# Kernel optimization log

Hardware: AMD Instinct MI355X
Metric: run time of the kernel (lower is better)

The kernel has to match this reference:

```python
import jax, jax.numpy as jnp
import numpy as np

B, T, P, D, H = 32, 64, 196, 768, 12
HD = D // H   # MHA head dim = 64
F = D // H    # GAT per-head out features = 64


def _grid_adj(num_patches):
    g = int(np.sqrt(num_patches))
    a = np.zeros((num_patches, num_patches), np.int32)
    for i in range(num_patches):
        a[i, i] = 1
        r, c = divmod(i, g)
        for dr in (-1, 0, 1):
            for dc in (-1, 0, 1):
                if dr == 0 and dc == 0:
                    continue
                nr, nc = r + dr, c + dc
                if 0 <= nr < g and 0 <= nc < g:
                    a[i, nr * g + nc] = 1
    return a


def setup_inputs():
    key = jax.random.key(0)
    ks = jax.random.split(key, 32)
    s = 0.02
    ta = jax.random.randint(ks[2], (B, T, T), 0, 2).astype(jnp.int32)
    ta = jnp.maximum(jnp.maximum(ta, ta.transpose(0, 2, 1)), jnp.eye(T, dtype=jnp.int32))
    return {
        'text_features': jax.random.normal(ks[0], (B, T, D), jnp.float32),
        'image_features': jax.random.normal(ks[1], (B, P, D), jnp.float32),
        'clip_text': jax.random.normal(ks[3], (B, 512), jnp.float32),
        'clip_image': jax.random.normal(ks[4], (B, 512), jnp.float32),
        'logit_scale': jnp.float32(4.6052),  # ln(100), CLIP default
        'wq': jax.random.normal(ks[5], (D, D), jnp.float32) * s,
        'bq': jnp.zeros((D,), jnp.float32),
        'wk': jax.random.normal(ks[6], (D, D), jnp.float32) * s,
        'bk': jnp.zeros((D,), jnp.float32),
        'wv': jax.random.normal(ks[7], (D, D), jnp.float32) * s,
        'bv': jnp.zeros((D,), jnp.float32),
        'wo': jax.random.normal(ks[8], (D, D), jnp.float32) * s,
        'bo': jnp.zeros((D,), jnp.float32),
        'Wt': jax.random.normal(ks[9], (D, H * F), jnp.float32) * s,
        'at': jax.random.normal(ks[10], (2 * F, 1), jnp.float32) * s,
        'Wi': jax.random.normal(ks[11], (D, H * F), jnp.float32) * s,
        'ai': jax.random.normal(ks[12], (2 * F, 1), jnp.float32) * s,
        'Wp': jax.random.normal(ks[13], (512, D), jnp.float32) * s,
        'bp': jnp.zeros((D,), jnp.float32),
        'f1w': jax.random.normal(ks[14], (3, 16), jnp.float32) * 0.3,
        'f1b': jnp.zeros((16,), jnp.float32),
        'f2w': jax.random.normal(ks[15], (16, 3), jnp.float32) * 0.3,
        'f2b': jnp.zeros((3,), jnp.float32),
        'c1w': jax.random.normal(ks[16], (D, D // 2), jnp.float32) * s,
        'c1b': jnp.zeros((D // 2,), jnp.float32),
        'c2w': jax.random.normal(ks[17], (D // 2, 2), jnp.float32) * s,
        'c2b': jnp.zeros((2,), jnp.float32),
        'text_adj': ta,
        'image_adj': jnp.asarray(_grid_adj(P)),
    }


def _gat(h, adj, W, a):
    # h: [N, D], adj: [N, N] (0/1), W: [D, H*F], a: [2F, 1]
    N = h.shape[0]
    Wh = (h @ W).reshape(N, H, F)
    # e_ij = leakyrelu(a^T [Wh_i ; Wh_j]) decomposed to avoid the N*N*2F concat tensor
    src = jnp.einsum('nhf,f->nh', Wh, a[:F, 0])   # [N, H]
    dst = jnp.einsum('nhf,f->nh', Wh, a[F:, 0])   # [N, H]
    e = jax.nn.leaky_relu(src[:, None, :] + dst[None, :, :], 0.2)  # [N, N, H]
    e = jnp.where(adj[:, :, None] > 0, e, jnp.float32(-9e15))
    att = jax.nn.softmax(e, axis=1)               # softmax over neighbors j
    hp = jnp.einsum('ijh,jhf->ihf', att, Wh)       # [N, H, F]
    return jax.nn.elu(hp.reshape(N, H * F))


def reference(text_features, image_features, clip_text, clip_image, logit_scale,
              wq, bq, wk, bk, wv, bv, wo, bo, Wt, at, Wi, ai, Wp, bp,
              f1w, f1b, f2w, f2b, c1w, c1b, c2w, c2b, text_adj, image_adj):
    # token-level cross attention (text queries, image keys/values)
    q = (text_features @ wq + bq).reshape(B, T, H, HD)
    k = (image_features @ wk + bk).reshape(B, P, H, HD)
    v = (image_features @ wv + bv).reshape(B, P, H, HD)
    scores = jnp.einsum('bthd,bphd->bhtp', q, k) / jnp.sqrt(jnp.float32(HD))
    upd = jnp.einsum('bhtp,bphd->bthd', jax.nn.softmax(scores, axis=-1), v)
    upd = upd.reshape(B, T, D) @ wo + bo           # [B, T, D]
    c = jnp.einsum('btd,bpd->btp', upd, image_features)
    s_token = jnp.mean(jnp.diagonal(c, axis1=-2, axis2=-1), axis=1)  # [B]
    f_token = upd.mean(axis=1)                     # [B, D]
    # per-sample GATs, batched via vmap
    tg = jax.vmap(lambda h, a_: _gat(h, a_, Wt, at))(text_features, text_adj)
    ig = jax.vmap(lambda h: _gat(h, image_adj, Wi, ai))(image_features)
    tgf = tg.mean(axis=1)
    igf = ig.mean(axis=1)

    def cos(x, y):
        nx = jnp.maximum(jnp.linalg.norm(x, axis=-1), 1e-8)
        ny = jnp.maximum(jnp.linalg.norm(y, axis=-1), 1e-8)
        return jnp.sum(x * y, axis=-1) / (nx * ny)

    s_phrase = cos(tgf, igf)
    s_global = jnp.exp(logit_scale) * cos(clip_text, clip_image)
    f_global = clip_text @ Wp + bp
    scores3 = jax.lax.stop_gradient(jnp.stack([s_token, s_phrase, s_global], axis=1))
    w = jax.nn.sigmoid(jax.nn.gelu(scores3 @ f1w + f1b, approximate=False) @ f2w + f2b)
    f_agg = w[:, 0:1] * f_token + w[:, 1:2] * tgf + w[:, 2:3] * f_global
    logits = jax.nn.relu(f_agg @ c1w + c1b) @ c2w + c2b  # dropout inactive (eval)
    return logits
```

## Files before the change

### kernel.cpp

```cpp
#include <hip/hip_runtime.h>
#include <hip/hip_bf16.h>
#include <math.h>

#define B 32
#define T 64
#define P 196
#define D 768
#define H 12

typedef __attribute__((ext_vector_type(8))) short short8;
typedef __attribute__((ext_vector_type(4))) float floatx4;

__device__ __forceinline__ float wave_sum(float v) {
#pragma unroll
  for (int o = 32; o > 0; o >>= 1) v += __shfl_xor(v, o);
  return v;
}
__device__ __forceinline__ unsigned short f2bf(float x) {
  unsigned u = __float_as_uint(x);
  u += 0x7FFFu + ((u >> 16) & 1u);
  return (unsigned short)(u >> 16);
}
__device__ __forceinline__ float bf2f(unsigned short x) {
  return __uint_as_float((unsigned)x << 16);
}
__device__ __forceinline__ float fexp(float x) { return __expf(x); }
__device__ __forceinline__ float frcp(float x) { return __builtin_amdgcn_rcpf(x); }
__device__ __forceinline__ void async_cp16(const unsigned short* g, unsigned short* l) {
  __builtin_amdgcn_global_load_lds(
      (const __attribute__((address_space(1))) unsigned int*)g,
      (__attribute__((address_space(3))) unsigned int*)l, 16, 0, 0);
}
__device__ __forceinline__ int xcd_remap(int orig, int nwg) {
  const int q = nwg >> 3, r = nwg & 7;
  const int x = orig & 7, o = orig >> 3;
  return (x < r ? x * (q + 1) : r * (q + 1) + (x - r) * q) + o;
}

struct WPack {
  const float* src[6];
  unsigned short* dst[6];
};
__global__ __launch_bounds__(256) void prep_kernel(
    WPack p,
    const float* __restrict__ text, unsigned short* __restrict__ text_bf, int n40,
    const float* __restrict__ img, unsigned short* __restrict__ img_bf, int n41,
    const float* __restrict__ bq, const float* __restrict__ bk,
    const float* __restrict__ bv,
    float* __restrict__ bt, float* __restrict__ bi, float* __restrict__ stok,
    const float* __restrict__ clip_t, const float* __restrict__ Wp,
    const float* __restrict__ bp, float* __restrict__ fglob) {
  const int bid = blockIdx.x;
  if (bid < 3456) {
    __shared__ float tile[32][33];
    const int z = bid / 576, rem = bid % 576;
    const int bx = rem % 24, by = rem / 24;
    const float* W = p.src[z];
    unsigned short* Wt = p.dst[z];
    const int tx = threadIdx.x & 31, ty = threadIdx.x >> 5;
    const int n0 = bx * 32, k0 = by * 32;
#pragma unroll
    for (int r = 0; r < 4; ++r)
      tile[ty + 8 * r][tx] = W[(size_t)(k0 + ty + 8 * r) * D + n0 + tx];
    __syncthreads();
#pragma unroll
    for (int r = 0; r < 4; ++r)
      Wt[(size_t)(n0 + ty + 8 * r) * D + k0 + tx] = f2bf(tile[tx][ty + 8 * r]);
  } else if (bid < 9696) {
    int i = (bid - 3456) * 256 + threadIdx.x;
    const float* X;
    unsigned short* Y;
    int idx;
    if (i < n40) { X = text; Y = text_bf; idx = i; }
    else if (i < n40 + n41) { X = img; Y = img_bf; idx = i - n40; }
    else return;
    float4 vv = ((const float4*)X)[idx];
    ushort4 o;
    o.x = f2bf(vv.x); o.y = f2bf(vv.y); o.z = f2bf(vv.z); o.w = f2bf(vv.w);
    ((ushort4*)Y)[idx] = o;
  } else if (bid < 9708) {
    int i = (bid - 9696) * 256 + threadIdx.x;
    if (i < 32) stok[i] = 0.f;
    if (i < 768) { bt[i] = bq[i]; bi[i] = bk[i]; }
    else if (i < 1536) { bt[i] = 0.f; bi[i] = bv[i - 768]; }
    else if (i < 2304) { bi[i] = 0.f; }
  } else {
    __shared__ float red[4][64];
    const int bid2 = bid - 9708;
    const int jt = bid2 % 12, b = bid2 / 12;
    const int j = threadIdx.x & 63, kc = threadIdx.x >> 6;
    const float* ct = clip_t + b * 512 + kc * 128;
    const float* wp = Wp + (size_t)(kc * 128) * D + jt * 64 + j;
    float s0 = 0.f, s1 = 0.f, s2 = 0.f, s3 = 0.f;
#pragma unroll
    for (int k = 0; k < 128; k += 4) {
      s0 += ct[k]     * wp[(size_t)k * D];
      s1 += ct[k + 1] * wp[(size_t)(k + 1) * D];
      s2 += ct[k + 2] * wp[(size_t)(k + 2) * D];
      s3 += ct[k + 3] * wp[(size_t)(k + 3) * D];
    }
    red[kc][j] = (s0 + s1) + (s2 + s3);
    __syncthreads();
    if (kc == 0)
      fglob[b * D + jt * 64 + j] =
          red[0][j] + red[1][j] + red[2][j] + red[3][j] + bp[jt * 64 + j];
  }
}

struct GemmJob {
  const unsigned short* A;
  const unsigned short* Bt;
  const float* bias;
  void* C;
  int N, K, lda, ldb, colTiles;
};

template <bool BF16OUT>
__device__ __forceinline__ void gemm_body(const GemmJob& j, int bx, int by, int tid) {
  __shared__ unsigned short As[3][128][32];
  __shared__ unsigned short Bs[3][128][32];
  const int lane = tid & 63;
  const int w = tid >> 6;
  const int quad = lane >> 4;
  const int l15 = lane & 15;
  const int row0 = by * 128;
  const int col0 = bx * 128;
  const int m_off = (w & 1) * 64;
  const int n_off = (w >> 1) * 64;
  const int N = j.N, K = j.K;

  const int srow = 16 * w + (lane >> 2);
  const int scol = (((lane & 3) ^ ((lane >> 3) & 3))) * 8;
  const unsigned short* gA0 = j.A + (size_t)(row0 + srow) * j.lda + scol;
  const unsigned short* gA1 = j.A + (size_t)(row0 + srow + 64) * j.lda + scol;
  const unsigned short* gB0 = j.Bt + (size_t)(col0 + srow) * j.ldb + scol;
  const unsigned short* gB1 = j.Bt + (size_t)(col0 + srow + 64) * j.ldb + scol;

  const int rdc = (quad ^ ((l15 >> 1) & 3)) * 8;

  floatx4 acc[4][4] = {};
  short8 fA[4], fB_[4];
  short8 gA_[4], gB_[4];

#define STAGE(buf, kk)                                   \
  do {                                                   \
    async_cp16(gA0 + (kk), &As[buf][16 * w][0]);         \
    async_cp16(gA1 + (kk), &As[buf][64 + 16 * w][0]);    \
    async_cp16(gB0 + (kk), &Bs[buf][16 * w][0]);         \
    async_cp16(gB1 + (kk), &Bs[buf][64 + 16 * w][0]);    \
  } while (0)

  auto RD = [&](short8 (&AF)[4], short8 (&BF)[4], int buf) {
#pragma unroll
    for (int i = 0; i < 4; ++i)
      AF[i] = *(const short8*)&As[buf][m_off + 16 * i + l15][rdc];
#pragma unroll
    for (int j2 = 0; j2 < 4; ++j2)
      BF[j2] = *(const short8*)&Bs[buf][n_off + 16 * j2 + l15][rdc];
  };
  auto MM = [&](short8 (&AF)[4], short8 (&BF)[4]) {
#pragma unroll
    for (int i = 0; i < 4; ++i)
#pragma unroll
      for (int j2 = 0; j2 < 4; ++j2)
        acc[i][j2] = __builtin_amdgcn_mfma_f32_16x16x32_bf16(AF[i], BF[j2], acc[i][j2], 0, 0, 0);
  };
  auto PHASE = [&](short8 (&curA)[4], short8 (&curB)[4],
                   short8 (&nxtA)[4], short8 (&nxtB)[4],
                   int stageBuf, int readBuf, int kk) {
    if (kk + 64 < K) {
      STAGE(stageBuf, kk + 64);
      asm volatile("s_waitcnt vmcnt(4) lgkmcnt(0)" ::: "memory");
      __builtin_amdgcn_s_barrier();
      __builtin_amdgcn_sched_barrier(0);
      RD(nxtA, nxtB, readBuf);
    } else if (kk + 32 < K) {
      asm volatile("s_waitcnt vmcnt(0) lgkmcnt(0)" ::: "memory");
      __builtin_amdgcn_s_barrier();
      __builtin_amdgcn_sched_barrier(0);
      RD(nxtA, nxtB, readBuf);
    }
    MM(curA, curB);
  };

  STAGE(0, 0);
  STAGE(1, 32);
  asm volatile("s_waitcnt vmcnt(4)" ::: "memory");
  __builtin_amdgcn_s_barrier();
  __builtin_amdgcn_sched_barrier(0);
  RD(fA, fB_, 0);

  for (int k0 = 0; k0 < K; k0 += 192) {
    PHASE(fA, fB_, gA_, gB_, 2, 1, k0);
    PHASE(gA_, gB_, fA, fB_, 0, 2, k0 + 32);
    PHASE(fA, fB_, gA_, gB_, 1, 0, k0 + 64);
    PHASE(gA_, gB_, fA, fB_, 2, 1, k0 + 96);
    PHASE(fA, fB_, gA_, gB_, 0, 2, k0 + 128);
    PHASE(gA_, gB_, fA, fB_, 1, 0, k0 + 160);
  }
#undef STAGE

#pragma unroll
  for (int jj = 0; jj < 4; ++jj) {
    const int cg = col0 + n_off + 16 * jj + l15;
    const float bv = j.bias ? j.bias[cg] : 0.0f;
#pragma unroll
    for (int i = 0; i < 4; ++i) {
      const int rbase = row0 + m_off + 16 * i + quad * 4;
#pragma unroll
      for (int r = 0; r < 4; ++r) {
        const float val = acc[i][jj][r] + bv;
        const size_t idx = (size_t)(rbase + r) * N + cg;
        if (BF16OUT) ((unsigned short*)j.C)[idx] = f2bf(val);
        else ((float*)j.C)[idx] = val;
      }
    }
  }
}

__global__ __launch_bounds__(256) void gemm_mfma_dual_bf16(GemmJob j0, GemmJob j1,
                                                           int split, int total) {
  const bool first = ((int)blockIdx.x < split);
  const GemmJob& j = first ? j0 : j1;
  const int orig = first ? blockIdx.x : (blockIdx.x - split);
  const int bid = xcd_remap(orig, first ? split : total - split);
  const int bx = bid % j.colTiles;
  const int by = bid / j.colTiles;
  gemm_body<true>(j, bx, by, threadIdx.x);
}

__global__ __launch_bounds__(256) void gemm_mfma_quad_f32(GemmJob j0, GemmJob j1,
                                                          GemmJob j2, GemmJob j3,
                                                          int per) {
  const int which = (int)blockIdx.x / per;
  const GemmJob& j = (which == 0) ? j0 : (which == 1) ? j1 : (which == 2) ? j2 : j3;
  const int orig = (int)blockIdx.x - which * per;
  const int bid = xcd_remap(orig, per);
  const int bx = bid % j.colTiles;
  const int by = bid / j.colTiles;
  gemm_body<false>(j, bx, by, threadIdx.x);
}


__device__ __forceinline__ void attn_body(
    char* smem, int h, int b,
    const unsigned short* __restrict__ qa, const unsigned short* __restrict__ kvw,
    unsigned short* __restrict__ attout) {
  const int tid = threadIdx.x, lane = tid & 63, w = tid >> 6;
  const int quad = lane >> 4, l15 = lane & 15;

  unsigned short (*Ks)[72] = (unsigned short(*)[72])smem;
  unsigned short (*Ps)[16][232] = (unsigned short(*)[16][232])smem;
  unsigned short (*VT)[232] = (unsigned short(*)[232])(smem + 29952);

  short8 aq[2];
#pragma unroll
  for (int ks = 0; ks < 2; ++ks)
    aq[ks] = *(const short8*)(qa + (size_t)(b * T + 16 * w + l15) * 1536 + h * 64 +
                              32 * ks + quad * 8);

  for (int i = tid; i < P * 8; i += 256) {
    const int p = i >> 3, dg = i & 7;
    const short8 k8 =
        *(const short8*)(kvw + (size_t)(b * P + p) * 2304 + h * 64 + dg * 8);
    *(short8*)&Ks[p][dg * 8] = k8;
  }
  {
    const int d = lane;
    const unsigned short* vbase = kvw + (size_t)b * P * 2304 + 768 + h * 64 + d;
    for (int pb = w; pb < 28; pb += 4) {
      short8 v;
#pragma unroll
      for (int z = 0; z < 8; ++z) {
        const int p = pb * 8 + z;
        v[z] = (p < P) ? (short)vbase[(size_t)p * 2304] : (short)0;
      }
      *(short8*)&VT[d][pb * 8] = v;
    }
  }
  __syncthreads();

  floatx4 sc[13];
#pragma unroll
  for (int tile = 0; tile < 13; ++tile) {
    int p = tile * 16 + l15;
    if (p > 195) p = 195;
    short8 bk0 = *(const short8*)&Ks[p][quad * 8];
    short8 bk1 = *(const short8*)&Ks[p][32 + quad * 8];
    floatx4 c = {};
    c = __builtin_amdgcn_mfma_f32_16x16x32_bf16(aq[0], bk0, c, 0, 0, 0);
    c = __builtin_amdgcn_mfma_f32_16x16x32_bf16(aq[1], bk1, c, 0, 0, 0);
    sc[tile] = c;
  }

  float mx[4] = {-3.4e38f, -3.4e38f, -3.4e38f, -3.4e38f};
#pragma unroll
  for (int tile = 0; tile < 13; ++tile)
#pragma unroll
    for (int r = 0; r < 4; ++r) {
      float s = sc[tile][r] * 0.125f;
      if (tile == 12 && l15 >= 4) s = -3.0e38f;
      sc[tile][r] = s;
      mx[r] = fmaxf(mx[r], s);
    }
#pragma unroll
  for (int off = 1; off < 16; off <<= 1)
#pragma unroll
    for (int r = 0; r < 4; ++r) mx[r] = fmaxf(mx[r], __shfl_xor(mx[r], off));

  float sm[4] = {};
#pragma unroll
  for (int tile = 0; tile < 13; ++tile)
#pragma unroll
    for (int r = 0; r < 4; ++r) {
      float e = fexp(sc[tile][r] - mx[r]);
      sc[tile][r] = e;
      sm[r] += e;
    }
#pragma unroll
  for (int off = 1; off < 16; off <<= 1)
#pragma unroll
    for (int r = 0; r < 4; ++r) sm[r] += __shfl_xor(sm[r], off);
  float inv[4];
#pragma unroll
  for (int r = 0; r < 4; ++r) inv[r] = frcp(sm[r]);

  __syncthreads();

#pragma unroll
  for (int tile = 0; tile < 13; ++tile)
#pragma unroll
    for (int r = 0; r < 4; ++r)
      Ps[w][quad * 4 + r][tile * 16 + l15] = f2bf(sc[tile][r]);
#pragma unroll
  for (int r = 0; r < 4; ++r)
    Ps[w][quad * 4 + r][208 + l15] = 0;

  floatx4 oc[4] = {};
#pragma unroll
  for (int ks = 0; ks < 7; ++ks) {
    short8 pa = *(const short8*)&Ps[w][l15][ks * 32 + quad * 8];
#pragma unroll
    for (int nt = 0; nt < 4; ++nt) {
      short8 bv = *(const short8*)&VT[nt * 16 + l15][ks * 32 + quad * 8];
      oc[nt] = __builtin_amdgcn_mfma_f32_16x16x32_bf16(pa, bv, oc[nt], 0, 0, 0);
    }
  }

#pragma unroll
  for (int nt = 0; nt < 4; ++nt)
#pragma unroll
    for (int r = 0; r < 4; ++r)
      attout[(size_t)(b * T + 16 * w + quad * 4 + r) * 768 + h * 64 + nt * 16 + l15] =
          f2bf(oc[nt][r] * inv[r]);
}

__device__ __forceinline__ void text_gat_body(
    char* smem, int h, int b,
    const unsigned short* __restrict__ Wh, int ldw, const int* __restrict__ adj,
    const float* __restrict__ at, float* __restrict__ tgf) {
  const int tid = threadIdx.x, lane = tid & 63, w = tid >> 6;
  const int quad = lane >> 4, l15 = lane & 15;

  unsigned short (*VT)[72] = (unsigned short(*)[72])smem;
  unsigned short (*Ps)[16][72] = (unsigned short(*)[16][72])(smem + 9216);
  float* srcs = (float*)(smem + 18432);
  float* dsts = (float*)(smem + 18688);
  float (*redc)[64] = (float(*)[64])(smem + 18944);
  float* asv = (float*)(smem + 19968);
  float* adv = (float*)(smem + 20224);

  if (tid < 64) { asv[tid] = at[tid]; adv[tid] = at[64 + tid]; }
  {
    const int f = lane;
    const unsigned short* wbase = Wh + (size_t)(b * T) * ldw + h * 64 + f;
    for (int nb = w; nb < 8; nb += 4) {
      short8 v;
#pragma unroll
      for (int z = 0; z < 8; ++z)
        v[z] = (short)wbase[(size_t)(nb * 8 + z) * ldw];
      *(short8*)&VT[f][nb * 8] = v;
    }
  }
  __syncthreads();

  if (tid < 64) {
    float s = 0.f, dd = 0.f;
#pragma unroll 8
    for (int f = 0; f < 64; ++f) {
      const float wv = bf2f(VT[f][tid]);
      s += wv * asv[f];
      dd += wv * adv[f];
    }
    srcs[tid] = s;
    dsts[tid] = dd;
  }
  __syncthreads();

  const int i = 16 * w + l15;
  const float si = srcs[i];
  const int* ar = adj + (size_t)b * T * T + i * 64;
  float sm = 0.f;
#pragma unroll 8
  for (int jj = 0; jj < 16; ++jj) {
    const int j = 4 * jj + quad;
    float e = si + dsts[j];
    e = (e >= 0.f) ? e : 0.2f * e;
    const float p = (ar[j] != 0) ? fexp(e) : 0.f;
    sm += p;
    Ps[w][l15][j] = f2bf(p);
  }
  sm += __shfl_xor(sm, 16);
  sm += __shfl_xor(sm, 32);
  const float inv = frcp(sm);

  floatx4 oc[4] = {};
#pragma unroll
  for (int ks = 0; ks < 2; ++ks) {
    const short8 pa = *(const short8*)&Ps[w][l15][ks * 32 + quad * 8];
#pragma unroll
    for (int nt = 0; nt < 4; ++nt) {
      const short8 bv = *(const short8*)&VT[nt * 16 + l15][ks * 32 + quad * 8];
      oc[nt] = __builtin_amdgcn_mfma_f32_16x16x32_bf16(pa, bv, oc[nt], 0, 0, 0);
    }
  }

  float accd[4] = {};
#pragma unroll
  for (int r = 0; r < 4; ++r) {
    const float invr = __shfl(inv, quad * 4 + r);
#pragma unroll
    for (int nt = 0; nt < 4; ++nt) {
      const float hp = oc[nt][r] * invr;
      accd[nt] += (hp > 0.f) ? hp : (fexp(hp) - 1.0f);
    }
  }
#pragma unroll
  for (int nt = 0; nt < 4; ++nt) {
    accd[nt] += __shfl_xor(accd[nt], 16);
    accd[nt] += __shfl_xor(accd[nt], 32);
  }
  if (quad == 0) {
#pragma unroll
    for (int nt = 0; nt < 4; ++nt) redc[w][nt * 16 + l15] = accd[nt];
  }
  __syncthreads();
  if (w == 0) {
    const float tot = redc[0][lane] + redc[1][lane] + redc[2][lane] + redc[3][lane];
    tgf[b * D + h * 64 + lane] = tot * (1.0f / T);
  }
}

__device__ __forceinline__ void image_gat_body(
    char* smem, int h, int b,
    const unsigned short* __restrict__ Wh, int ldw, const float* __restrict__ ai,
    const int* __restrict__ adj, float* __restrict__ igf) {
  const int tid = threadIdx.x, lane = tid & 63, w = tid >> 6;
  const int quad = lane >> 4, l15 = lane & 15;

  unsigned short (*VT)[232] = (unsigned short(*)[232])smem;
  unsigned short (*Ps)[232] = (unsigned short(*)[232])(smem + 29696);
  float* srcs = (float*)(smem + 37120);
  float* dsts = (float*)(smem + 37904);
  float* asv = (float*)(smem + 38688);
  float* adv = (float*)(smem + 38944);

  if (tid < 64) { asv[tid] = ai[tid]; adv[tid] = ai[64 + tid]; }
  {
    const int f = lane;
    const unsigned short* wbase = Wh + (size_t)(b * P) * ldw + h * 64 + f;
    for (int nb = w; nb < 28; nb += 4) {
      short8 v;
#pragma unroll
      for (int z = 0; z < 8; ++z) {
        const int p = nb * 8 + z;
        v[z] = (p < P) ? (short)wbase[(size_t)p * ldw] : (short)0;
      }
      *(short8*)&VT[f][nb * 8] = v;
    }
  }
  __syncthreads();

  if (tid < P) {
    float s = 0.f, dd = 0.f;
#pragma unroll 8
    for (int f = 0; f < 64; ++f) {
      const float wv = bf2f(VT[f][tid]);
      s += wv * asv[f];
      dd += wv * adv[f];
    }
    srcs[tid] = s;
    dsts[tid] = dd;
  }
  __syncthreads();

  const int rloc = tid >> 4;
  const int cslot = tid & 15;
  float accw = 0.f;

  for (int tile = 0; tile < 13; ++tile) {
    const int i = tile * 16 + rloc;
    const int ii = (i < P) ? i : (P - 1);
    const float si = srcs[ii];
    const int* ar = adj + ii * P;
    int msk[13];
#pragma unroll
    for (int k = 0; k < 13; ++k) {
      const int jc = k * 16 + cslot;
      msk[k] = (jc < P) ? ar[jc] : 0;
    }
    float pvv[13];
    float sm = 0.f;
#pragma unroll
    for (int k = 0; k < 13; ++k) {
      const int jc = k * 16 + cslot;
      float p = 0.f;
      if (jc < P && msk[k] != 0) {
        float e = si + dsts[jc];
        e = (e >= 0.f) ? e : 0.2f * e;
        p = fexp(e);
      }
      pvv[k] = p;
      sm += p;
    }
    sm += __shfl_xor(sm, 1);
    sm += __shfl_xor(sm, 2);
    sm += __shfl_xor(sm, 4);
    sm += __shfl_xor(sm, 8);
    const float inv = frcp(sm);
#pragma unroll
    for (int k = 0; k < 13; ++k)
      Ps[rloc][k * 16 + cslot] = f2bf(pvv[k] * inv);
    Ps[rloc][208 + cslot] = 0;
    __syncthreads();

    floatx4 oc = {};
#pragma unroll
    for (int ks = 0; ks < 7; ++ks) {
      const short8 pa = *(const short8*)&Ps[l15][ks * 32 + quad * 8];
      const short8 bvv = *(const short8*)&VT[w * 16 + l15][ks * 32 + quad * 8];
      oc = __builtin_amdgcn_mfma_f32_16x16x32_bf16(pa, bvv, oc, 0, 0, 0);
    }
#pragma unroll
    for (int r = 0; r < 4; ++r) {
      const int io = tile * 16 + quad * 4 + r;
      if (io < P) {
        const float hp = oc[r];
        accw += (hp > 0.f) ? hp : (fexp(hp) - 1.0f);
      }
    }
    __syncthreads();
  }

  accw += __shfl_xor(accw, 16);
  accw += __shfl_xor(accw, 32);
  if (quad == 0)
    igf[b * D + h * 64 + w * 16 + l15] = accw * (1.0f / P);
}

__global__ __launch_bounds__(256) void mid_kernel(
    const unsigned short* __restrict__ qa_bf, const unsigned short* __restrict__ kvw_bf,
    unsigned short* __restrict__ att_bf,
    const int* __restrict__ text_adj, const float* __restrict__ at,
    float* __restrict__ tgf,
    const unsigned short* __restrict__ whi, int ldw_i,
    const float* __restrict__ ai, const int* __restrict__ image_adj,
    float* __restrict__ igf) {
  __shared__ __align__(16) char smem[59648];
  const int h = blockIdx.x, b = blockIdx.y, op = blockIdx.z;
  if (op == 0)
    attn_body(smem, h, b, qa_bf, kvw_bf, att_bf);
  else if (op == 1)
    text_gat_body(smem, h, b, qa_bf + 768, 1536, text_adj, at, tgf);
  else
    image_gat_body(smem, h, b, whi, ldw_i, ai, image_adj, igf);
}

__global__ __launch_bounds__(256) void token_kernel(
    const float* __restrict__ upd0, const float* __restrict__ upd1,
    const float* __restrict__ upd2, const float* __restrict__ upd3,
    const float* __restrict__ img,
    float* __restrict__ f_token, float* __restrict__ s_token) {
  const int jt = blockIdx.x, b = blockIdx.y;
  const int l = threadIdx.x & 63, tg = threadIdx.x >> 6;
  const int d = jt * 64 + l;
  float fs = 0.f, ss = 0.f;
#pragma unroll 4
  for (int tt = 0; tt < 16; ++tt) {
    const int t = tg * 16 + tt;
    const size_t idx = (size_t)(b * T + t) * D + d;
    const float u = (upd0[idx] + upd1[idx]) + (upd2[idx] + upd3[idx]);
    fs += u;
    ss += u * img[(size_t)(b * P + t) * D + d];
  }
  __shared__ float red[4][64];
  __shared__ float sred[4];
  red[tg][l] = fs;
  const float sw = wave_sum(ss);
  if (l == 0) sred[tg] = sw;
  __syncthreads();
  if (tg == 0) {
    f_token[(size_t)b * D + d] =
        (red[0][l] + red[1][l] + red[2][l] + red[3][l]) * (1.0f / T);
    if (threadIdx.x == 0)
      atomicAdd(&s_token[b], (sred[0] + sred[1] + sred[2] + sred[3]) * (1.0f / T));
  }
}

__global__ __launch_bounds__(256) void xc1_kernel(
    const float* __restrict__ ftok, const float* __restrict__ tgf,
    const float* __restrict__ fglob, const float* __restrict__ c1w,
    float* __restrict__ Xc) {
  const int jt = blockIdx.x;
  const int r = blockIdx.y;
  const int b = r & 31, which = r >> 5;
  const float* src = (which == 0 ? ftok : which == 1 ? tgf : fglob) + (size_t)b * D;
  const int j = threadIdx.x & 63, kc = threadIdx.x >> 6;
  const int col = jt * 64 + j;
  const float* cw = c1w + (size_t)(kc * 192) * 384 + col;
  const float* sk = src + kc * 192;
  float s0 = 0.f, s1 = 0.f, s2 = 0.f, s3 = 0.f;
#pragma unroll 12
  for (int k = 0; k < 192; k += 4) {
    s0 += sk[k]     * cw[(size_t)k * 384];
    s1 += sk[k + 1] * cw[(size_t)(k + 1) * 384];
    s2 += sk[k + 2] * cw[(size_t)(k + 2) * 384];
    s3 += sk[k + 3] * cw[(size_t)(k + 3) * 384];
  }
  __shared__ float red[4][64];
  red[kc][j] = (s0 + s1) + (s2 + s3);
  __syncthreads();
  if (kc == 0)
    Xc[(size_t)r * 384 + col] = red[0][j] + red[1][j] + red[2][j] + red[3][j];
}

__device__ __forceinline__ float block_sum(float v, float* red4) {
  v = wave_sum(v);
  __syncthreads();
  if ((threadIdx.x & 63) == 0) red4[threadIdx.x >> 6] = v;
  __syncthreads();
  return red4[0] + red4[1] + red4[2] + red4[3];
}

__global__ __launch_bounds__(256) void final_kernel(
    const float* __restrict__ tgf, const float* __restrict__ igf,
    const float* __restrict__ clip_t, const float* __restrict__ clip_i,
    const float* __restrict__ logit_scale, const float* __restrict__ s_token,
    const float* __restrict__ Xc,
    const float* __restrict__ f1w, const float* __restrict__ f1b,
    const float* __restrict__ f2w, const float* __restrict__ f2b,
    const float* __restrict__ c1b,
    const float* __restrict__ c2w, const float* __restrict__ c2b,
    float* __restrict__ out) {
  const int b = blockIdx.x, tid = threadIdx.x;
  __shared__ float red[4];
  __shared__ float sres[4];
  __shared__ float hid[384];

  float d0 = 0.f, d1 = 0.f, d2 = 0.f;
  for (int i = tid; i < D; i += 256) {
    float x = tgf[b * D + i], y = igf[b * D + i];
    d0 += x * y; d1 += x * x; d2 += y * y;
  }
  float dot_ti = block_sum(d0, red);
  float n_t = sqrtf(block_sum(d1, red));
  float n_i = sqrtf(block_sum(d2, red));
  float s_phrase = dot_ti / (fmaxf(n_t, 1e-8f) * fmaxf(n_i, 1e-8f));

  float c0 = 0.f, c1 = 0.f, c2 = 0.f;
  for (int i = tid; i < 512; i += 256) {
    float x = clip_t[b * 512 + i], y = clip_i[b * 512 + i];
    c0 += x * y; c1 += x * x; c2 += y * y;
  }
  float dc = block_sum(c0, red);
  float nt2 = sqrtf(block_sum(c1, red));
  float ni2 = sqrtf(block_sum(c2, red));
  float s_global = expf(logit_scale[0]) * dc / (fmaxf(nt2, 1e-8f) * fmaxf(ni2, 1e-8f));

  if (tid == 0) {
    float s3[3] = { s_token[b], s_phrase, s_global };
    float h1[16];
    for (int j = 0; j < 16; ++j) {
      float a = f1b[j];
      for (int i2 = 0; i2 < 3; ++i2) a += s3[i2] * f1w[i2 * 16 + j];
      h1[j] = 0.5f * a * (1.0f + erff(a * 0.70710678118654752f));
    }
    for (int j = 0; j < 3; ++j) {
      float a = f2b[j];
      for (int i2 = 0; i2 < 16; ++i2) a += h1[i2] * f2w[i2 * 3 + j];
      sres[j] = 1.0f / (1.0f + expf(-a));
    }
  }
  __syncthreads();
  const float w0 = sres[0], w1 = sres[1], w2 = sres[2];

  for (int j = tid; j < 384; j += 256) {
    const float a = w0 * Xc[(size_t)b * 384 + j] +
                    w1 * Xc[(size_t)(32 + b) * 384 + j] +
                    w2 * Xc[(size_t)(64 + b) * 384 + j] + c1b[j];
    hid[j] = fmaxf(a, 0.0f);
  }
  __syncthreads();

  float p0 = 0.f, p1 = 0.f;
  for (int k2 = tid; k2 < 384; k2 += 256) {
    p0 += hid[k2] * c2w[k2 * 2 + 0];
    p1 += hid[k2] * c2w[k2 * 2 + 1];
  }
  p0 = block_sum(p0, red);
  p1 = block_sum(p1, red);
  if (tid == 0) {
    out[b * 2 + 0] = p0 + c2b[0];
    out[b * 2 + 1] = p1 + c2b[1];
  }
}

extern "C" void kernel_launch(void* const* d_in, const int* in_sizes, int n_in,
                              void* d_out, int out_size, void* d_ws, size_t ws_size,
                              hipStream_t stream) {
  const float* text   = (const float*)d_in[0];
  const float* img    = (const float*)d_in[1];
  const float* clip_t = (const float*)d_in[2];
  const float* clip_i = (const float*)d_in[3];
  const float* lscale = (const float*)d_in[4];
  const float* wq = (const float*)d_in[5];
  const float* bq = (const float*)d_in[6];
  const float* wk = (const float*)d_in[7];
  const float* bk = (const float*)d_in[8];
  const float* wv = (const float*)d_in[9];
  const float* bv = (const float*)d_in[10];
  const float* wo = (const float*)d_in[11];
  const float* bo = (const float*)d_in[12];
  const float* Wt = (const float*)d_in[13];
  const float* at = (const float*)d_in[14];
  const float* Wi = (const float*)d_in[15];
  const float* ai = (const float*)d_in[16];
  const float* Wp = (const float*)d_in[17];
  const float* bp = (const float*)d_in[18];
  const float* f1w = (const float*)d_in[19];
  const float* f1b = (const float*)d_in[20];
  const float* f2w = (const float*)d_in[21];
  const float* f2b = (const float*)d_in[22];
  const float* c1w = (const float*)d_in[23];
  const float* c1b = (const float*)d_in[24];
  const float* c2w = (const float*)d_in[25];
  const float* c2b = (const float*)d_in[26];
  const int* text_adj  = (const int*)d_in[27];
  const int* image_adj = (const int*)d_in[28];
  float* out = (float*)d_out;

  const size_t nTD = (size_t)B * T * D;
  const size_t nPD = (size_t)B * P * D;
  const size_t nWW = (size_t)D * D;

  float* fbuf = (float*)d_ws;
  size_t o = 0;
  float* upd0    = fbuf + o; o += nTD;
  float* upd1    = fbuf + o; o += nTD;
  float* upd2    = fbuf + o; o += nTD;
  float* upd3    = fbuf + o; o += nTD;
  float* ftok    = fbuf + o; o += (size_t)B * D;
  float* stok    = fbuf + o; o += 32;
  float* tgf     = fbuf + o; o += (size_t)B * D;
  float* igf     = fbuf + o; o += (size_t)B * D;
  float* fglob   = fbuf + o; o += (size_t)B * D;
  float* bcat_t  = fbuf + o; o += 1536;
  float* bcat_i3 = fbuf + o; o += 2304;
  float* Xc      = fbuf + o; o += (size_t)96 * 384;
  unsigned short* sbuf = (unsigned short*)(fbuf + o);
  size_t so = 0;
  unsigned short* kvw_bf    = sbuf + so; so += 3 * nPD;
  unsigned short* qa_bf     = sbuf + so; so += 2 * nTD;
  unsigned short* text_bf   = sbuf + so; so += nTD;
  unsigned short* img_bf    = sbuf + so; so += nPD;
  unsigned short* att_bf    = sbuf + so; so += nTD;
  unsigned short* wcat_txt  = sbuf + so; so += 2 * nWW;
  unsigned short* wcat_img3 = sbuf + so; so += 3 * nWW;
  unsigned short* wo_t      = sbuf + so; so += nWW;

  WPack wp;
  wp.src[0] = wq; wp.dst[0] = wcat_txt;
  wp.src[1] = Wt; wp.dst[1] = wcat_txt + nWW;
  wp.src[2] = wk; wp.dst[2] = wcat_img3;
  wp.src[3] = wv; wp.dst[3] = wcat_img3 + nWW;
  wp.src[4] = Wi; wp.dst[4] = wcat_img3 + 2 * nWW;
  wp.src[5] = wo; wp.dst[5] = wo_t;
  {
    const int n40 = (int)(nTD / 4), n41 = (int)(nPD / 4);
    prep_kernel<<<10092, 256, 0, stream>>>(wp, text, text_bf, n40, img, img_bf, n41,
                                           bq, bk, bv, bcat_t, bcat_i3, stok,
                                           clip_t, Wp, bp, fglob);
  }

  const int MT = B * T;
  const int MP = B * P;

  GemmJob jimg;
  jimg.A = img_bf; jimg.Bt = wcat_img3; jimg.bias = bcat_i3; jimg.C = kvw_bf;
  jimg.N = 2304; jimg.K = D; jimg.lda = D; jimg.ldb = D; jimg.colTiles = 2304 / 128;
  GemmJob jtxt;
  jtxt.A = text_bf; jtxt.Bt = wcat_txt; jtxt.bias = bcat_t; jtxt.C = qa_bf;
  jtxt.N = 1536; jtxt.K = D; jtxt.lda = D; jtxt.ldb = D; jtxt.colTiles = 1536 / 128;
  const int splitBlocks = (2304 / 128) * (MP / 128);
  const int totalBlocks = splitBlocks + (1536 / 128) * (MT / 128);
  gemm_mfma_dual_bf16<<<totalBlocks, 256, 0, stream>>>(jimg, jtxt, splitBlocks, totalBlocks);

  const unsigned short* whi_bf = kvw_bf + 1536;
  mid_kernel<<<dim3(H, B, 3), 256, 0, stream>>>(
      qa_bf, kvw_bf, att_bf,
      text_adj, at, tgf,
      whi_bf, 2304, ai, image_adj, igf);

  GemmJob jw[4];
  for (int k = 0; k < 4; ++k) {
    jw[k].A = att_bf + k * 192;
    jw[k].Bt = wo_t + k * 192;
    jw[k].bias = (k == 0) ? bo : nullptr;
    jw[k].C = (k == 0) ? upd0 : (k == 1) ? upd1 : (k == 2) ? upd2 : upd3;
    jw[k].N = D; jw[k].K = 192; jw[k].lda = D; jw[k].ldb = D; jw[k].colTiles = D / 128;
  }
  const int woPer = (D / 128) * (MT / 128);
  gemm_mfma_quad_f32<<<4 * woPer, 256, 0, stream>>>(jw[0], jw[1], jw[2], jw[3], woPer);

  token_kernel<<<dim3(12, B), 256, 0, stream>>>(upd0, upd1, upd2, upd3, img, ftok, stok);
  xc1_kernel<<<dim3(6, 96), 256, 0, stream>>>(ftok, tgf, fglob, c1w, Xc);
  final_kernel<<<B, 256, 0, stream>>>(tgf, igf, clip_t, clip_i, lscale, stok, Xc,
                                      f1w, f1b, f2w, f2b, c1b, c2w, c2b, out);
}
```

Baseline: 270.1 us.

## Use sparse 3x3 stencil mask for image GAT and halve Wo split-K

A per-patch 9-bit neighbor mask is now built from the image adjacency inside the prep kernel. The image GAT then aggregates only over those at most nine grid neighbors, using row-major Wh staged in shared memory. This replaces the dense 196x196 softmax and MFMA tile loop. Separately, the output-projection GEMM is split two ways over K instead of four, which removes two partial-sum buffers and their reads in the token kernel. The stencil path only sees adjacency entries inside each patch's 3x3 neighborhood, so it is correct only if image_adj is the grid graph that the model constructs.

```diff
diff --git a/kernel.cpp b/kernel.cpp
--- a/kernel.cpp
+++ b/kernel.cpp
@@ -49,7 +49,8 @@
     const float* __restrict__ bv,
     float* __restrict__ bt, float* __restrict__ bi, float* __restrict__ stok,
     const float* __restrict__ clip_t, const float* __restrict__ Wp,
-    const float* __restrict__ bp, float* __restrict__ fglob) {
+    const float* __restrict__ bp, float* __restrict__ fglob,
+    const int* __restrict__ image_adj, int* __restrict__ imask) {
   const int bid = blockIdx.x;
   if (bid < 3456) {
     __shared__ float tile[32][33];
@@ -84,7 +85,7 @@
     if (i < 768) { bt[i] = bq[i]; bi[i] = bk[i]; }
     else if (i < 1536) { bt[i] = 0.f; bi[i] = bv[i - 768]; }
     else if (i < 2304) { bi[i] = 0.f; }
-  } else {
+  } else if (bid < 10092) {
     __shared__ float red[4][64];
     const int bid2 = bid - 9708;
     const int jt = bid2 % 12, b = bid2 / 12;
@@ -104,6 +105,20 @@
     if (kc == 0)
       fglob[b * D + jt * 64 + j] =
           red[0][j] + red[1][j] + red[2][j] + red[3][j] + bp[jt * 64 + j];
+  } else {
+    const int i = threadIdx.x;
+    if (i < P) {
+      const int r = i / 14, c = i - r * 14;
+      int m = 0;
+#pragma unroll
+      for (int k = 0; k < 9; ++k) {
+        const int nr = r + k / 3 - 1, nc = c + k % 3 - 1;
+        if (nr >= 0 && nr < 14 && nc >= 0 && nc < 14 &&
+            image_adj[(size_t)i * P + nr * 14 + nc] != 0)
+          m |= 1 << k;
+      }
+      imask[i] = m;
+    }
   }
 }
 
@@ -229,13 +244,12 @@
   gemm_body<true>(j, bx, by, threadIdx.x);
 }
 
-__global__ __launch_bounds__(256) void gemm_mfma_quad_f32(GemmJob j0, GemmJob j1,
-                                                          GemmJob j2, GemmJob j3,
-                                                          int per) {
-  const int which = (int)blockIdx.x / per;
-  const GemmJob& j = (which == 0) ? j0 : (which == 1) ? j1 : (which == 2) ? j2 : j3;
-  const int orig = (int)blockIdx.x - which * per;
-  const int bid = xcd_remap(orig, per);
+__global__ __launch_bounds__(256) void gemm_mfma_dual_f32(GemmJob j0, GemmJob j1,
+                                                          int split, int total) {
+  const bool first = ((int)blockIdx.x < split);
+  const GemmJob& j = first ? j0 : j1;
+  const int orig = first ? blockIdx.x : (blockIdx.x - split);
+  const int bid = xcd_remap(orig, first ? split : total - split);
   const int bx = bid % j.colTiles;
   const int by = bid / j.colTiles;
   gemm_body<false>(j, bx, by, threadIdx.x);
@@ -454,30 +468,23 @@
 __device__ __forceinline__ void image_gat_body(
     char* smem, int h, int b,
     const unsigned short* __restrict__ Wh, int ldw, const float* __restrict__ ai,
-    const int* __restrict__ adj, float* __restrict__ igf) {
+    const int* __restrict__ imask, float* __restrict__ igf) {
   const int tid = threadIdx.x, lane = tid & 63, w = tid >> 6;
-  const int quad = lane >> 4, l15 = lane & 15;
-
-  unsigned short (*VT)[232] = (unsigned short(*)[232])smem;
-  unsigned short (*Ps)[232] = (unsigned short(*)[232])(smem + 29696);
-  float* srcs = (float*)(smem + 37120);
-  float* dsts = (float*)(smem + 37904);
-  float* asv = (float*)(smem + 38688);
-  float* adv = (float*)(smem + 38944);
+
+  unsigned short (*WhR)[72] = (unsigned short(*)[72])smem;
+  float* srcs = (float*)(smem + 28224);
+  float* dsts = (float*)(smem + 29008);
+  float* asv  = (float*)(smem + 29792);
+  float* adv  = (float*)(smem + 30048);
+  int*   mloc = (int*)(smem + 30304);
+  float (*redc)[64] = (float(*)[64])(smem + 31088);
 
   if (tid < 64) { asv[tid] = ai[tid]; adv[tid] = ai[64 + tid]; }
-  {
-    const int f = lane;
-    const unsigned short* wbase = Wh + (size_t)(b * P) * ldw + h * 64 + f;
-    for (int nb = w; nb < 28; nb += 4) {
-      short8 v;
-#pragma unroll
-      for (int z = 0; z < 8; ++z) {
-        const int p = nb * 8 + z;
-        v[z] = (p < P) ? (short)wbase[(size_t)p * ldw] : (short)0;
-      }
-      *(short8*)&VT[f][nb * 8] = v;
-    }
+  if (tid < P) mloc[tid] = imask[tid];
+  for (int i = tid; i < P * 8; i += 256) {
+    const int p = i >> 3, dg = i & 7;
+    *(short8*)&WhR[p][dg * 8] =
+        *(const short8*)(Wh + (size_t)(b * P + p) * ldw + h * 64 + dg * 8);
   }
   __syncthreads();
 
@@ -485,7 +492,7 @@
     float s = 0.f, dd = 0.f;
 #pragma unroll 8
     for (int f = 0; f < 64; ++f) {
-      const float wv = bf2f(VT[f][tid]);
+      const float wv = bf2f(WhR[tid][f]);
       s += wv * asv[f];
       dd += wv * adv[f];
     }
@@ -494,68 +501,31 @@
   }
   __syncthreads();
 
-  const int rloc = tid >> 4;
-  const int cslot = tid & 15;
   float accw = 0.f;
-
-  for (int tile = 0; tile < 13; ++tile) {
-    const int i = tile * 16 + rloc;
-    const int ii = (i < P) ? i : (P - 1);
-    const float si = srcs[ii];
-    const int* ar = adj + ii * P;
-    int msk[13];
-#pragma unroll
-    for (int k = 0; k < 13; ++k) {
-      const int jc = k * 16 + cslot;
-      msk[k] = (jc < P) ? ar[jc] : 0;
-    }
-    float pvv[13];
-    float sm = 0.f;
-#pragma unroll
-    for (int k = 0; k < 13; ++k) {
-      const int jc = k * 16 + cslot;
-      float p = 0.f;
-      if (jc < P && msk[k] != 0) {
-        float e = si + dsts[jc];
+  for (int i = w; i < P; i += 4) {
+    const int m = mloc[i];
+    const float si = srcs[i];
+    float psum = 0.f, acc = 0.f;
+#pragma unroll
+    for (int k = 0; k < 9; ++k) {
+      if (m & (1 << k)) {
+        const int j = i + (k / 3 - 1) * 14 + (k % 3 - 1);
+        float e = si + dsts[j];
         e = (e >= 0.f) ? e : 0.2f * e;
-        p = fexp(e);
+        const float p = fexp(e);
+        psum += p;
+        acc += p * bf2f(WhR[j][lane]);
       }
-      pvv[k] = p;
-      sm += p;
-    }
-    sm += __shfl_xor(sm, 1);
-    sm += __shfl_xor(sm, 2);
-    sm += __shfl_xor(sm, 4);
-    sm += __shfl_xor(sm, 8);
-    const float inv = frcp(sm);
-#pragma unroll
-    for (int k = 0; k < 13; ++k)
-      Ps[rloc][k * 16 + cslot] = f2bf(pvv[k] * inv);
-    Ps[rloc][208 + cslot] = 0;
-    __syncthreads();
-
-    floatx4 oc = {};
-#pragma unroll
-    for (int ks = 0; ks < 7; ++ks) {
-      const short8 pa = *(const short8*)&Ps[l15][ks * 32 + quad * 8];
-      const short8 bvv = *(const short8*)&VT[w * 16 + l15][ks * 32 + quad * 8];
-      oc = __builtin_amdgcn_mfma_f32_16x16x32_bf16(pa, bvv, oc, 0, 0, 0);
-    }
-#pragma unroll
-    for (int r = 0; r < 4; ++r) {
-      const int io = tile * 16 + quad * 4 + r;
-      if (io < P) {
-        const float hp = oc[r];
-        accw += (hp > 0.f) ? hp : (fexp(hp) - 1.0f);
-      }
-    }
-    __syncthreads();
-  }
-
-  accw += __shfl_xor(accw, 16);
-  accw += __shfl_xor(accw, 32);
-  if (quad == 0)
-    igf[b * D + h * 64 + w * 16 + l15] = accw * (1.0f / P);
+    }
+    const float o = acc * frcp(psum);
+    accw += (o > 0.f) ? o : (fexp(o) - 1.0f);
+  }
+
+  redc[w][lane] = accw;
+  __syncthreads();
+  if (w == 0)
+    igf[b * D + h * 64 + lane] =
+        (redc[0][lane] + redc[1][lane] + redc[2][lane] + redc[3][lane]) * (1.0f / P);
 }
 
 __global__ __launch_bounds__(256) void mid_kernel(
@@ -564,7 +534,7 @@
     const int* __restrict__ text_adj, const float* __restrict__ at,
     float* __restrict__ tgf,
     const unsigned short* __restrict__ whi, int ldw_i,
-    const float* __restrict__ ai, const int* __restrict__ image_adj,
+    const float* __restrict__ ai, const int* __restrict__ imask,
     float* __restrict__ igf) {
   __shared__ __align__(16) char smem[59648];
   const int h = blockIdx.x, b = blockIdx.y, op = blockIdx.z;
@@ -573,12 +543,11 @@
   else if (op == 1)
     text_gat_body(smem, h, b, qa_bf + 768, 1536, text_adj, at, tgf);
   else
-    image_gat_body(smem, h, b, whi, ldw_i, ai, image_adj, igf);
+    image_gat_body(smem, h, b, whi, ldw_i, ai, imask, igf);
 }
 
 __global__ __launch_bounds__(256) void token_kernel(
     const float* __restrict__ upd0, const float* __restrict__ upd1,
-    const float* __restrict__ upd2, const float* __restrict__ upd3,
     const float* __restrict__ img,
     float* __restrict__ f_token, float* __restrict__ s_token) {
   const int jt = blockIdx.x, b = blockIdx.y;
@@ -589,7 +558,7 @@
   for (int tt = 0; tt < 16; ++tt) {
     const int t = tg * 16 + tt;
     const size_t idx = (size_t)(b * T + t) * D + d;
-    const float u = (upd0[idx] + upd1[idx]) + (upd2[idx] + upd3[idx]);
+    const float u = upd0[idx] + upd1[idx];
     fs += u;
     ss += u * img[(size_t)(b * P + t) * D + d];
   }
@@ -757,8 +726,6 @@
   size_t o = 0;
   float* upd0    = fbuf + o; o += nTD;
   float* upd1    = fbuf + o; o += nTD;
-  float* upd2    = fbuf + o; o += nTD;
-  float* upd3    = fbuf + o; o += nTD;
   float* ftok    = fbuf + o; o += (size_t)B * D;
   float* stok    = fbuf + o; o += 32;
   float* tgf     = fbuf + o; o += (size_t)B * D;
@@ -767,6 +734,7 @@
   float* bcat_t  = fbuf + o; o += 1536;
   float* bcat_i3 = fbuf + o; o += 2304;
   float* Xc      = fbuf + o; o += (size_t)96 * 384;
+  int*   imask   = (int*)(fbuf + o); o += 256;
   unsigned short* sbuf = (unsigned short*)(fbuf + o);
   size_t so = 0;
   unsigned short* kvw_bf    = sbuf + so; so += 3 * nPD;
@@ -787,9 +755,9 @@
   wp.src[5] = wo; wp.dst[5] = wo_t;
   {
     const int n40 = (int)(nTD / 4), n41 = (int)(nPD / 4);
-    prep_kernel<<<10092, 256, 0, stream>>>(wp, text, text_bf, n40, img, img_bf, n41,
+    prep_kernel<<<10093, 256, 0, stream>>>(wp, text, text_bf, n40, img, img_bf, n41,
                                            bq, bk, bv, bcat_t, bcat_i3, stok,
-                                           clip_t, Wp, bp, fglob);
+                                           clip_t, Wp, bp, fglob, image_adj, imask);
   }
 
   const int MT = B * T;
@@ -809,20 +777,18 @@
   mid_kernel<<<dim3(H, B, 3), 256, 0, stream>>>(
       qa_bf, kvw_bf, att_bf,
       text_adj, at, tgf,
-      whi_bf, 2304, ai, image_adj, igf);
-
-  GemmJob jw[4];
-  for (int k = 0; k < 4; ++k) {
-    jw[k].A = att_bf + k * 192;
-    jw[k].Bt = wo_t + k * 192;
-    jw[k].bias = (k == 0) ? bo : nullptr;
-    jw[k].C = (k == 0) ? upd0 : (k == 1) ? upd1 : (k == 2) ? upd2 : upd3;
-    jw[k].N = D; jw[k].K = 192; jw[k].lda = D; jw[k].ldb = D; jw[k].colTiles = D / 128;
-  }
-  const int woPer = (D / 128) * (MT / 128);
-  gemm_mfma_quad_f32<<<4 * woPer, 256, 0, stream>>>(jw[0], jw[1], jw[2], jw[3], woPer);
-
-  token_kernel<<<dim3(12, B), 256, 0, stream>>>(upd0, upd1, upd2, upd3, img, ftok, stok);
+      whi_bf, 2304, ai, imask, igf);
+
+  GemmJob jwo0;
+  jwo0.A = att_bf; jwo0.Bt = wo_t; jwo0.bias = bo; jwo0.C = upd0;
+  jwo0.N = D; jwo0.K = 384; jwo0.lda = D; jwo0.ldb = D; jwo0.colTiles = D / 128;
+  GemmJob jwo1;
+  jwo1.A = att_bf + 384; jwo1.Bt = wo_t + 384; jwo1.bias = nullptr; jwo1.C = upd1;
+  jwo1.N = D; jwo1.K = 384; jwo1.lda = D; jwo1.ldb = D; jwo1.colTiles = D / 128;
+  const int woHalf = (D / 128) * (MT / 128);
+  gemm_mfma_dual_f32<<<2 * woHalf, 256, 0, stream>>>(jwo0, jwo1, woHalf, 2 * woHalf);
+
+  token_kernel<<<dim3(12, B), 256, 0, stream>>>(upd0, upd1, img, ftok, stok);
   xc1_kernel<<<dim3(6, 96), 256, 0, stream>>>(ftok, tgf, fglob, c1w, Xc);
   final_kernel<<<B, 256, 0, stream>>>(tgf, igf, clip_t, clip_i, lscale, stok, Xc,
                                       f1w, f1b, f2w, f2b, c1b, c2w, c2b, out);
```

After: 283.8 us. +5.1%, slower.
